# Performance work log

Hardware: AMD Instinct MI355X
Metric: run time of the kernel (lower is better)

## Reference

```python
import jax, jax.numpy as jnp
import numpy as np

B = 16384
S0, S1 = 7, 7
NB, NC = 2, 20
WC, WN = 5.0, 0.5  # weight_coord, weight_noobject
D = NB * 5 + NC  # 30


def setup_inputs() -> dict:
    key = jax.random.key(0)
    k1, k2, k3, k4 = jax.random.split(key, 4)
    predication = jax.random.normal(k1, (B, S0 * S1 * D), dtype=jnp.float32)
    grid = jax.random.randint(k2, (B, S0, S1), 0, 2, dtype=jnp.int32)
    tbox = jax.random.uniform(k3, (B, S0, S1, 4), dtype=jnp.float32)
    # keep target w,h strictly positive (real boxes), offsets in [0,1)
    tbox = tbox.at[..., 2:].set(0.05 + 0.9 * tbox[..., 2:])
    tcls = jax.random.randint(k4, (B, S0, S1), 0, NC, dtype=jnp.int32)
    return {"predication": predication, "grid": grid, "tbox": tbox, "tcls": tcls}


def _yolo_loss(predication, grid, tbox, tcls):
    pred = predication.reshape(B, S0, S1, D)
    conf = jax.nn.sigmoid(pred[..., :NB])                                  # (B,S0,S1,NB)
    pb = jax.nn.sigmoid(pred[..., NB:5 * NB]).reshape(B, S0, S1, NB, 4)    # (B,S0,S1,NB,4)
    cls = jax.nn.softmax(pred[..., 5 * NB:], axis=-1)                      # (B,S0,S1,NC)

    # cell coordinates: x = column index, y = row index (matches the [1,0] swap in torch code)
    xg = jnp.arange(S1, dtype=pred.dtype)[None, None, :]   # (1,1,S1)
    yg = jnp.arange(S0, dtype=pred.dtype)[None, :, None]   # (1,S0,1)

    tox, toy, tw, th = tbox[..., 0], tbox[..., 1], tbox[..., 2], tbox[..., 3]
    tcx = (xg + tox) / S0
    tcy = (yg + toy) / S1

    pcx = (xg[..., None] + pb[..., 0]) / S0   # (B,S0,S1,NB)
    pcy = (yg[..., None] + pb[..., 1]) / S1
    pw, ph = pb[..., 2], pb[..., 3]

    # IOU of each predicted box vs the cell's target box (same formula as _calc_iou)
    tb_ = jnp.minimum(tcx[..., None] + tw[..., None] / 2, pcx + pw / 2) - \
          jnp.maximum(tcx[..., None] - tw[..., None] / 2, pcx - pw / 2)
    lr_ = jnp.minimum(tcy[..., None] + th[..., None] / 2, pcy + ph / 2) - \
          jnp.maximum(tcy[..., None] - th[..., None] / 2, pcy - ph / 2)
    inter = jnp.where((tb_ < 0) | (lr_ < 0), 0.0, tb_ * lr_)
    iou = inter / ((tw * th)[..., None] + pw * ph - inter)                 # (B,S0,S1,NB)

    # best predictor chosen on detached IOUs (original uses pred_boxes.detach())
    best = jnp.argmax(jax.lax.stop_gradient(iou), axis=-1)                 # (B,S0,S1)

    take = lambda a: jnp.take_along_axis(a, best[..., None], axis=-1)[..., 0]
    iou_b = take(iou)          # attached IOU re-used in confidence loss
    conf_b = take(conf)
    pbb = jnp.take_along_axis(pb, best[..., None, None], axis=3)[..., 0, :]  # (B,S0,S1,4)

    cls_t = jnp.take_along_axis(cls, tcls[..., None], axis=-1)[..., 0]

    coord = (pbb[..., 0] - tox) ** 2 + (pbb[..., 1] - toy) ** 2 \
          + (jnp.sqrt(pbb[..., 2]) - jnp.sqrt(tw)) ** 2 \
          + (jnp.sqrt(pbb[..., 3]) - jnp.sqrt(th)) ** 2

    obj_loss = WC * coord + (conf_b - iou_b) ** 2 + (1.0 - cls_t) ** 2     # (B,S0,S1)
    noobj_loss = WN * jnp.sum(conf ** 2, axis=-1)                          # (B,S0,S1)

    objm = (grid == 1).astype(pred.dtype)
    total = jnp.sum(objm * obj_loss + (1.0 - objm) * noobj_loss)
    return total / B


def reference(predication, grid, tbox, tcls):
    return _yolo_loss(predication, grid, tbox, tcls)
```

## Files before the change

### kernel.cpp

```cpp
#include <hip/hip_runtime.h>
#include <math.h>

namespace {

constexpr int kB    = 16384;
constexpr int kS0   = 7;
constexpr int kS1   = 7;
constexpr int kD    = 30;
constexpr int kCells = kB * kS0 * kS1;
constexpr int TPB   = 256;
constexpr int NBLK  = kCells / TPB;
constexpr int F4PB  = TPB * kD / 4;
constexpr float kInv7 = 1.0f / 7.0f;
constexpr float kWC = 5.0f;
constexpr float kWN = 0.5f;

__device__ __forceinline__ float sigm(float x) {
    return 1.0f / (1.0f + __expf(-x));
}

__global__ void zero_out(float* out) {
    if (threadIdx.x == 0) out[0] = 0.0f;
}

__global__ void __launch_bounds__(TPB) yolo_loss_kernel(
    const float* __restrict__ pred,
    const int*   __restrict__ grid,
    const float* __restrict__ tbox,
    const int*   __restrict__ tcls,
    float* __restrict__ out)
{
    __shared__ float sp[TPB * kD];
    __shared__ float wsum[TPB / 64];

    const int tid   = threadIdx.x;
    const int cell0 = blockIdx.x * TPB;
    const int cell  = cell0 + tid;
    const int wave  = tid >> 6;
    const int lane  = tid & 63;

    const float4* __restrict__ g4 =
        reinterpret_cast<const float4*>(pred + (size_t)cell0 * kD);
    float4* s4 = reinterpret_cast<float4*>(sp);

    float4 r[7];
    #pragma unroll
    for (int k = 0; k < 7; ++k) r[k] = g4[tid + 256 * k];
    float4 r7;
    const bool extra = (tid < F4PB - 256 * 7);
    if (extra) r7 = g4[256 * 7 + tid];

    const float4 tb4 = reinterpret_cast<const float4*>(tbox)[cell];
    const int g  = grid[cell];
    const int tc = tcls[cell];

    #pragma unroll
    for (int k = 0; k < 7; ++k) s4[tid + 256 * k] = r[k];
    if (extra) s4[256 * 7 + tid] = r7;
    __syncthreads();

    const int cj = cell % kS1;
    const int ci = (cell / kS1) % kS0;

    float f[kD];
    {
        const float2* p2 = reinterpret_cast<const float2*>(sp + tid * kD);
        #pragma unroll
        for (int q = 0; q < kD / 2; ++q) {
            float2 t = p2[q];
            f[2 * q]     = t.x;
            f[2 * q + 1] = t.y;
        }
    }

    const float tox = tb4.x, toy = tb4.y, tw = tb4.z, th = tb4.w;

    const float conf0 = sigm(f[0]);
    const float conf1 = sigm(f[1]);
    float pbx[2], pby[2], pbw[2], pbh[2];
    #pragma unroll
    for (int k = 0; k < 2; ++k) {
        pbx[k] = sigm(f[2 + 4 * k + 0]);
        pby[k] = sigm(f[2 + 4 * k + 1]);
        pbw[k] = sigm(f[2 + 4 * k + 2]);
        pbh[k] = sigm(f[2 + 4 * k + 3]);
    }

    float cmax = f[10];
    #pragma unroll
    for (int q = 11; q < 30; ++q) cmax = fmaxf(cmax, f[q]);
    float csum = 0.0f, et = 0.0f;
    #pragma unroll
    for (int q = 0; q < 20; ++q) {
        const float e = __expf(f[10 + q] - cmax);
        csum += e;
        et = (q == tc) ? e : et;
    }
    const float cls_t = et / csum;

    const float x = (float)cj, y = (float)ci;
    const float tcx = (x + tox) * kInv7;
    const float tcy = (y + toy) * kInv7;
    const float thw = tw * 0.5f, thh = th * 0.5f;
    const float tarea = tw * th;

    float iou0, iou1;
    {
        const float pcx = (x + pbx[0]) * kInv7;
        const float pcy = (y + pby[0]) * kInv7;
        const float pw = pbw[0], ph = pbh[0];
        const float tb_ = fminf(tcx + thw, pcx + pw * 0.5f) - fmaxf(tcx - thw, pcx - pw * 0.5f);
        const float lr_ = fminf(tcy + thh, pcy + ph * 0.5f) - fmaxf(tcy - thh, pcy - ph * 0.5f);
        float inter = tb_ * lr_;
        inter = (tb_ < 0.0f || lr_ < 0.0f) ? 0.0f : inter;
        iou0 = inter / (tarea + pw * ph - inter);
    }
    {
        const float pcx = (x + pbx[1]) * kInv7;
        const float pcy = (y + pby[1]) * kInv7;
        const float pw = pbw[1], ph = pbh[1];
        const float tb_ = fminf(tcx + thw, pcx + pw * 0.5f) - fmaxf(tcx - thw, pcx - pw * 0.5f);
        const float lr_ = fminf(tcy + thh, pcy + ph * 0.5f) - fmaxf(tcy - thh, pcy - ph * 0.5f);
        float inter = tb_ * lr_;
        inter = (tb_ < 0.0f || lr_ < 0.0f) ? 0.0f : inter;
        iou1 = inter / (tarea + pw * ph - inter);
    }

    const bool b1 = (iou1 > iou0);
    const float bx = b1 ? pbx[1] : pbx[0];
    const float by = b1 ? pby[1] : pby[0];
    const float bw = b1 ? pbw[1] : pbw[0];
    const float bh = b1 ? pbh[1] : pbh[0];
    const float conf_b = b1 ? conf1 : conf0;
    const float iou_b  = b1 ? iou1  : iou0;

    const float dx = bx - tox;
    const float dy = by - toy;
    const float dw = sqrtf(bw) - sqrtf(tw);
    const float dh = sqrtf(bh) - sqrtf(th);
    const float coord = dx * dx + dy * dy + dw * dw + dh * dh;
    const float d1 = conf_b - iou_b;
    const float d2 = 1.0f - cls_t;
    const float obj   = kWC * coord + d1 * d1 + d2 * d2;
    const float noobj = kWN * (conf0 * conf0 + conf1 * conf1);

    float v = (g == 1) ? obj : noobj;

    #pragma unroll
    for (int off = 32; off > 0; off >>= 1) v += __shfl_down(v, off, 64);
    if (lane == 0) wsum[wave] = v;
    __syncthreads();
    if (tid == 0) {
        atomicAdd(out, (wsum[0] + wsum[1] + wsum[2] + wsum[3]) * (1.0f / kB));
    }
}

}

extern "C" void kernel_launch(void* const* d_in, const int* in_sizes, int n_in,
                              void* d_out, int out_size, void* d_ws, size_t ws_size,
                              hipStream_t stream) {
    const float* pred = (const float*)d_in[0];
    const int*   grid = (const int*)d_in[1];
    const float* tbox = (const float*)d_in[2];
    const int*   tcls = (const int*)d_in[3];
    float* out = (float*)d_out;

    zero_out<<<1, 64, 0, stream>>>(out);
    yolo_loss_kernel<<<NBLK, TPB, 0, stream>>>(pred, grid, tbox, tcls, out);
}
```

Before: 169.0 us.

## Use single-wave blocks and spread atomics over 64 partial slots

Blocks shrink from 256 threads to one 64-lane wave, so the second __syncthreads and the shared-memory cross-wave reduction go away. Each block atomically adds its sum into one of 64 workspace slots instead of a single output word, which spreads atomic contention. A memset clears the slots and a small finishing kernel adds them and scales by 1/B. The catch is four times as many blocks and atomics, plus an extra launch.

```diff
diff --git a/kernel.cpp b/kernel.cpp
--- a/kernel.cpp
+++ b/kernel.cpp
@@ -8,9 +8,9 @@
 constexpr int kS1   = 7;
 constexpr int kD    = 30;
 constexpr int kCells = kB * kS0 * kS1;
-constexpr int TPB   = 256;
+constexpr int TPB   = 64;
 constexpr int NBLK  = kCells / TPB;
-constexpr int F4PB  = TPB * kD / 4;
+constexpr int NSLOT = 64;
 constexpr float kInv7 = 1.0f / 7.0f;
 constexpr float kWC = 5.0f;
 constexpr float kWN = 0.5f;
@@ -19,25 +19,18 @@
     return 1.0f / (1.0f + __expf(-x));
 }
 
-__global__ void zero_out(float* out) {
-    if (threadIdx.x == 0) out[0] = 0.0f;
-}
-
-__global__ void __launch_bounds__(TPB) yolo_loss_kernel(
+__global__ void yolo_loss_kernel(
     const float* __restrict__ pred,
     const int*   __restrict__ grid,
     const float* __restrict__ tbox,
     const int*   __restrict__ tcls,
-    float* __restrict__ out)
+    float* __restrict__ partials)
 {
     __shared__ float sp[TPB * kD];
-    __shared__ float wsum[TPB / 64];
 
     const int tid   = threadIdx.x;
     const int cell0 = blockIdx.x * TPB;
     const int cell  = cell0 + tid;
-    const int wave  = tid >> 6;
-    const int lane  = tid & 63;
 
     const float4* __restrict__ g4 =
         reinterpret_cast<const float4*>(pred + (size_t)cell0 * kD);
@@ -45,18 +38,18 @@
 
     float4 r[7];
     #pragma unroll
-    for (int k = 0; k < 7; ++k) r[k] = g4[tid + 256 * k];
+    for (int k = 0; k < 7; ++k) r[k] = g4[tid + 64 * k];
     float4 r7;
-    const bool extra = (tid < F4PB - 256 * 7);
-    if (extra) r7 = g4[256 * 7 + tid];
+    const bool extra = (tid < 32);
+    if (extra) r7 = g4[448 + tid];
 
     const float4 tb4 = reinterpret_cast<const float4*>(tbox)[cell];
     const int g  = grid[cell];
     const int tc = tcls[cell];
 
     #pragma unroll
-    for (int k = 0; k < 7; ++k) s4[tid + 256 * k] = r[k];
-    if (extra) s4[256 * 7 + tid] = r7;
+    for (int k = 0; k < 7; ++k) s4[tid + 64 * k] = r[k];
+    if (extra) s4[448 + tid] = r7;
     __syncthreads();
 
     const int cj = cell % kS1;
@@ -104,35 +97,26 @@
     const float thw = tw * 0.5f, thh = th * 0.5f;
     const float tarea = tw * th;
 
-    float iou0, iou1;
-    {
-        const float pcx = (x + pbx[0]) * kInv7;
-        const float pcy = (y + pby[0]) * kInv7;
-        const float pw = pbw[0], ph = pbh[0];
+    float iou[2];
+    #pragma unroll
+    for (int k = 0; k < 2; ++k) {
+        const float pcx = (x + pbx[k]) * kInv7;
+        const float pcy = (y + pby[k]) * kInv7;
+        const float pw = pbw[k], ph = pbh[k];
         const float tb_ = fminf(tcx + thw, pcx + pw * 0.5f) - fmaxf(tcx - thw, pcx - pw * 0.5f);
         const float lr_ = fminf(tcy + thh, pcy + ph * 0.5f) - fmaxf(tcy - thh, pcy - ph * 0.5f);
         float inter = tb_ * lr_;
         inter = (tb_ < 0.0f || lr_ < 0.0f) ? 0.0f : inter;
-        iou0 = inter / (tarea + pw * ph - inter);
-    }
-    {
-        const float pcx = (x + pbx[1]) * kInv7;
-        const float pcy = (y + pby[1]) * kInv7;
-        const float pw = pbw[1], ph = pbh[1];
-        const float tb_ = fminf(tcx + thw, pcx + pw * 0.5f) - fmaxf(tcx - thw, pcx - pw * 0.5f);
-        const float lr_ = fminf(tcy + thh, pcy + ph * 0.5f) - fmaxf(tcy - thh, pcy - ph * 0.5f);
-        float inter = tb_ * lr_;
-        inter = (tb_ < 0.0f || lr_ < 0.0f) ? 0.0f : inter;
-        iou1 = inter / (tarea + pw * ph - inter);
+        iou[k] = inter / (tarea + pw * ph - inter);
     }
 
-    const bool b1 = (iou1 > iou0);
+    const bool b1 = (iou[1] > iou[0]);
     const float bx = b1 ? pbx[1] : pbx[0];
     const float by = b1 ? pby[1] : pby[0];
     const float bw = b1 ? pbw[1] : pbw[0];
     const float bh = b1 ? pbh[1] : pbh[0];
     const float conf_b = b1 ? conf1 : conf0;
-    const float iou_b  = b1 ? iou1  : iou0;
+    const float iou_b  = b1 ? iou[1] : iou[0];
 
     const float dx = bx - tox;
     const float dy = by - toy;
@@ -148,11 +132,18 @@
 
     #pragma unroll
     for (int off = 32; off > 0; off >>= 1) v += __shfl_down(v, off, 64);
-    if (lane == 0) wsum[wave] = v;
-    __syncthreads();
     if (tid == 0) {
-        atomicAdd(out, (wsum[0] + wsum[1] + wsum[2] + wsum[3]) * (1.0f / kB));
+        atomicAdd(&partials[blockIdx.x & (NSLOT - 1)], v);
     }
+}
+
+__global__ void finish_kernel(const float* __restrict__ partials,
+                              float* __restrict__ out)
+{
+    float v = partials[threadIdx.x];
+    #pragma unroll
+    for (int off = 32; off > 0; off >>= 1) v += __shfl_down(v, off, 64);
+    if (threadIdx.x == 0) out[0] = v * (1.0f / kB);
 }
 
 }
@@ -164,8 +155,10 @@
     const int*   grid = (const int*)d_in[1];
     const float* tbox = (const float*)d_in[2];
     const int*   tcls = (const int*)d_in[3];
-    float* out = (float*)d_out;
+    float* out      = (float*)d_out;
+    float* partials = (float*)d_ws;
 
-    zero_out<<<1, 64, 0, stream>>>(out);
-    yolo_loss_kernel<<<NBLK, TPB, 0, stream>>>(pred, grid, tbox, tcls, out);
+    hipMemsetAsync(partials, 0, NSLOT * sizeof(float), stream);
+    yolo_loss_kernel<<<NBLK, TPB, 0, stream>>>(pred, grid, tbox, tcls, partials);
+    finish_kernel<<<1, 64, 0, stream>>>(partials, out);
 }
```

Result: slower. 202.6 us (+19.9%).
